# Performance work log

Measured on AMD Instinct MI355X. Metric: run time of the kernel, lower is better.

## Reference

```python
import jax, jax.numpy as jnp
import numpy as np

TAU = 0.5
EPS = 1e-12  # torch F.normalize eps
N, HIDDEN, PROJ = 16384, 512, 128


def setup_inputs() -> dict:
    key = jax.random.key(0)
    k1, k2, k3, k4 = jax.random.split(key, 4)
    scale1 = 1.0 / np.sqrt(HIDDEN)
    scale2 = 1.0 / np.sqrt(PROJ)
    return {
        "z1": jax.random.normal(k1, (N, HIDDEN), dtype=jnp.float32),
        "z2": jax.random.normal(k2, (N, HIDDEN), dtype=jnp.float32),
        "W1": jax.random.normal(k3, (HIDDEN, PROJ), dtype=jnp.float32) * scale1,
        "b1": jnp.zeros((PROJ,), dtype=jnp.float32),
        "W2": jax.random.normal(k4, (PROJ, PROJ), dtype=jnp.float32) * scale2,
        "b2": jnp.zeros((PROJ,), dtype=jnp.float32),
    }


def _project(z, W1, b1, W2, b2):
    # GRACE projection head: Linear -> ELU -> Linear
    h = jax.nn.elu(z @ W1 + b1)
    return h @ W2 + b2


def _l2_normalize(x):
    nrm = jnp.sqrt(jnp.sum(x * x, axis=1, keepdims=True))
    return x / jnp.maximum(nrm, EPS)


def _semi_loss(u, v):
    nu = _l2_normalize(u)
    nv = _l2_normalize(v)
    intra = jnp.exp((nu @ nu.T) / TAU)  # [N, N]
    inter = jnp.exp((nu @ nv.T) / TAU)  # [N, N]
    pos = jnp.diagonal(inter)
    denom = intra.sum(axis=1) + inter.sum(axis=1) - jnp.diagonal(intra)
    return -jnp.log(pos / denom)


def reference(z1, z2, W1, b1, W2, b2):
    u = _project(z1, W1, b1, W2, b2)
    v = _project(z2, W1, b1, W2, b2)
    l1 = _semi_loss(u, v)
    l2 = _semi_loss(v, u)
    return jnp.mean((l1 + l2) * 0.5)
```

## Files before the change

kernel.cpp:

```cpp
#include <hip/hip_runtime.h>

#define NROWS 16384
#define M2    32768
#define TT    128
#define HID   512
#define PROJ  128

constexpr float SCALE_L2E = 2.8853900817779268f;
constexpr float E2        = 7.38905609893065f;

typedef float f32x2   __attribute__((ext_vector_type(2)));
typedef float f32x4   __attribute__((ext_vector_type(4)));
typedef short bf16x8  __attribute__((ext_vector_type(8)));
typedef int   i32x8   __attribute__((ext_vector_type(8)));

__device__ inline short f2bf(float x) {
  union { float f; unsigned u; } v; v.f = x;
  unsigned r = v.u + 0x7fffu + ((v.u >> 16) & 1u);
  return (short)(r >> 16);
}
__device__ inline float bf2f(short s) {
  union { unsigned u; float f; } v; v.u = ((unsigned)(unsigned short)s) << 16;
  return v.f;
}
__device__ inline unsigned char f2fp8(float x) {
  return (unsigned char)(__builtin_amdgcn_cvt_pk_fp8_f32(x, x, 0, false) & 0xff);
}
__device__ inline unsigned cvtpk_bf16(float a, float b) {
  unsigned r;
  asm("v_cvt_pk_bf16_f32 %0, %1, %2" : "=v"(r) : "v"(a), "v"(b));
  return r;
}

__global__ void kprep(const float* __restrict__ W1, const float* __restrict__ W2,
                      short* __restrict__ W1t, short* __restrict__ W2t) {
  int stride = gridDim.x * blockDim.x;
  for (int idx = blockIdx.x * blockDim.x + threadIdx.x; idx < 128 * 512; idx += stride) {
    int n = idx >> 9, k = idx & 511;
    W1t[idx] = f2bf(W1[k * 128 + n]);
  }
  for (int idx = blockIdx.x * blockDim.x + threadIdx.x; idx < 128 * 128; idx += stride) {
    int n = idx >> 7, k = idx & 127;
    W2t[idx] = f2bf(W2[k * 128 + n]);
  }
}

__global__ __launch_bounds__(256) void kproj(const float* __restrict__ z1,
                                             const float* __restrict__ z2,
                                             const short* __restrict__ W1t,
                                             const float* __restrict__ b1,
                                             const short* __restrict__ W2t,
                                             const float* __restrict__ b2,
                                             short* __restrict__ nn,
                                             unsigned char* __restrict__ nnf,
                                             unsigned char* __restrict__ nsf) {
  __shared__ short hls[64 * 128];
  int wave = threadIdx.x >> 6, lane = threadIdx.x & 63;
  int lr = lane & 15, lg = lane >> 4;
  const float* z = (blockIdx.x < 256) ? z1 : z2;
  int rloc = (blockIdx.x & 255) * 64 + wave * 16;
  int rglob0 = blockIdx.x * 64 + wave * 16;
  const float* zrow = z + (size_t)(rloc + lr) * HID;

  f32x4 acc[8];
#pragma unroll
  for (int ct = 0; ct < 8; ++ct) acc[ct] = (f32x4){0.f, 0.f, 0.f, 0.f};

  for (int kc = 0; kc < HID / 32; ++kc) {
    int kof = kc * 32 + lg * 8;
    f32x4 za = *(const f32x4*)(zrow + kof);
    f32x4 zb = *(const f32x4*)(zrow + kof + 4);
    union { unsigned u[4]; bf16x8 v; } af;
    af.u[0] = cvtpk_bf16(za[0], za[1]);
    af.u[1] = cvtpk_bf16(za[2], za[3]);
    af.u[2] = cvtpk_bf16(zb[0], zb[1]);
    af.u[3] = cvtpk_bf16(zb[2], zb[3]);
#pragma unroll
    for (int ct = 0; ct < 8; ++ct) {
      bf16x8 b = *(const bf16x8*)(W1t + (ct * 16 + lr) * HID + kof);
      acc[ct] = __builtin_amdgcn_mfma_f32_16x16x32_bf16(af.v, b, acc[ct], 0, 0, 0);
    }
  }
#pragma unroll
  for (int ct = 0; ct < 8; ++ct) {
    int col = ct * 16 + lr;
    float bias = b1[col];
#pragma unroll
    for (int q = 0; q < 4; ++q) {
      int lrow = wave * 16 + lg * 4 + q;
      float x = acc[ct][q] + bias;
      x = x > 0.f ? x : (__builtin_amdgcn_exp2f(x * 1.44269504088896f) - 1.0f);
      int sw = (col >> 3) ^ (lrow & 15);
      hls[lrow * 128 + sw * 8 + (col & 7)] = f2bf(x);
    }
  }
  __syncthreads();

  int lrow2 = wave * 16 + lr;
  f32x4 acc2[8];
#pragma unroll
  for (int ct = 0; ct < 8; ++ct) acc2[ct] = (f32x4){0.f, 0.f, 0.f, 0.f};

#pragma unroll
  for (int kc = 0; kc < PROJ / 32; ++kc) {
    bf16x8 a = *(const bf16x8*)&hls[lrow2 * 128 + (((kc * 4 + lg) ^ lr) << 3)];
#pragma unroll
    for (int ct = 0; ct < 8; ++ct) {
      bf16x8 b = *(const bf16x8*)(W2t + (ct * 16 + lr) * PROJ + kc * 32 + lg * 8);
      acc2[ct] = __builtin_amdgcn_mfma_f32_16x16x32_bf16(a, b, acc2[ct], 0, 0, 0);
    }
  }
#pragma unroll
  for (int ct = 0; ct < 8; ++ct) {
    float bias = b2[ct * 16 + lr];
#pragma unroll
    for (int q = 0; q < 4; ++q) acc2[ct][q] += bias;
  }
  float inv[4];
#pragma unroll
  for (int q = 0; q < 4; ++q) {
    float s = 0.f;
#pragma unroll
    for (int ct = 0; ct < 8; ++ct) s += acc2[ct][q] * acc2[ct][q];
    s += __shfl_xor(s, 1); s += __shfl_xor(s, 2);
    s += __shfl_xor(s, 4); s += __shfl_xor(s, 8);
    inv[q] = 1.f / fmaxf(sqrtf(s), 1e-12f);
  }
#pragma unroll
  for (int ct = 0; ct < 8; ++ct) {
    int col = ct * 16 + lr;
#pragma unroll
    for (int q = 0; q < 4; ++q) {
      int row = rglob0 + lg * 4 + q;
      float v = acc2[ct][q] * inv[q];
      nn[(size_t)row * PROJ + col]  = f2bf(v);
      nnf[(size_t)row * PROJ + col] = f2fp8(v);
      nsf[(size_t)row * PROJ + col] = f2fp8(v * SCALE_L2E);
    }
  }
}

__global__ __launch_bounds__(512, 4) void ksim13(const unsigned char* __restrict__ nnf,
                                                 const unsigned char* __restrict__ nsf,
                                                 float* __restrict__ d) {
  __shared__ long BtL[256 * 16];
  __shared__ float colbuf[8][256];

  int tid = threadIdx.x;
  int w = tid >> 6, lane = tid & 63;
  int lr = lane & 15, lg = lane >> 4;

  int t = blockIdx.x;
  float ff = (float)((2 * TT + 1) * (2 * TT + 1) - 8 * t);
  int ib = (int)(((float)(2 * TT + 1) - sqrtf(ff)) * 0.5f);
  if (ib < 0) ib = 0;
  if (ib > TT - 1) ib = TT - 1;
  while (ib > 0 && ib * (2 * TT - ib + 1) / 2 > t) --ib;
  while ((ib + 1) * (2 * TT - ib) / 2 <= t) ++ib;
  int jb = ib + (t - ib * (2 * TT - ib + 1) / 2);
  bool diag = (ib == jb);

  int i0 = ib * 256 + w * 32;

  i32x8 a[2];
#pragma unroll
  for (int rb = 0; rb < 2; ++rb)
    a[rb] = *(const i32x8*)(nsf + (size_t)(i0 + rb * 16 + lr) * PROJ + lg * 32);

  {
    int slot = tid & 15, row0 = tid >> 4;
    const long* bsrc = (const long*)(nnf + (size_t)(jb * 256 + row0) * PROJ) + slot;
    long st[8];
#pragma unroll
    for (int r = 0; r < 8; ++r) st[r] = bsrc[(size_t)r * 32 * 16];
#pragma unroll
    for (int r = 0; r < 8; ++r) {
      int row = r * 32 + row0;
      BtL[row * 16 + (slot ^ (row & 15))] = st[r];
    }
  }
  __syncthreads();

  f32x4 rs0 = (f32x4){0.f, 0.f, 0.f, 0.f};
  f32x4 rs1 = (f32x4){0.f, 0.f, 0.f, 0.f};

  const char* bb = (const char*)BtL + lr * 128;
  unsigned xo0 = (unsigned)(((lg * 4 + 0) ^ lr) << 3);
  unsigned xo1 = (unsigned)(((lg * 4 + 1) ^ lr) << 3);
  unsigned xo2 = (unsigned)(((lg * 4 + 2) ^ lr) << 3);
  unsigned xo3 = (unsigned)(((lg * 4 + 3) ^ lr) << 3);

  union BFrag { long h[4]; i32x8 v; };

  BFrag cur;
  cur.h[0] = *(const long*)(bb + xo0);
  cur.h[1] = *(const long*)(bb + xo1);
  cur.h[2] = *(const long*)(bb + xo2);
  cur.h[3] = *(const long*)(bb + xo3);

#pragma unroll 2
  for (int jt = 0; jt < 16; ++jt) {
    const char* bn = bb + 2048;
    BFrag nxt;
    nxt.h[0] = *(const long*)(bn + xo0);
    nxt.h[1] = *(const long*)(bn + xo1);
    nxt.h[2] = *(const long*)(bn + xo2);
    nxt.h[3] = *(const long*)(bn + xo3);

    f32x4 c0 = (f32x4){0.f, 0.f, 0.f, 0.f};
    f32x4 c1 = (f32x4){0.f, 0.f, 0.f, 0.f};
    c0 = __builtin_amdgcn_mfma_scale_f32_16x16x128_f8f6f4(a[0], cur.v, c0, 0, 0,
                                                          0, 0x7f7f7f7f, 0, 0x7f7f7f7f);
    c1 = __builtin_amdgcn_mfma_scale_f32_16x16x128_f8f6f4(a[1], cur.v, c1, 0, 0,
                                                          0, 0x7f7f7f7f, 0, 0x7f7f7f7f);

    f32x4 e0, e1;
#pragma unroll
    for (int q = 0; q < 4; ++q) {
      e0[q] = __builtin_amdgcn_exp2f(c0[q]);
      e1[q] = __builtin_amdgcn_exp2f(c1[q]);
    }
    rs0 += e0;
    rs1 += e1;
    f32x4 s4 = e0 + e1;
    f32x2 h2 = __builtin_shufflevector(s4, s4, 0, 1)
             + __builtin_shufflevector(s4, s4, 2, 3);
    float cs = h2[0] + h2[1];
    cs += __shfl_xor(cs, 16);
    cs += __shfl_xor(cs, 32);
    if (lg == 0) colbuf[w][jt * 16 + lr] = cs;

    cur = nxt;
    bb = bn;
  }

  float myval = 0.f;
#pragma unroll
  for (int rb = 0; rb < 2; ++rb)
#pragma unroll
    for (int q = 0; q < 4; ++q) {
      float v = (rb == 0) ? rs0[q] : rs1[q];
      v += __shfl_xor(v, 1); v += __shfl_xor(v, 2);
      v += __shfl_xor(v, 4); v += __shfl_xor(v, 8);
      if (lr == rb * 4 + q) myval = v;
    }
  if (lr < 8)
    atomicAdd(&d[i0 + (lr >> 2) * 16 + lg * 4 + (lr & 3)], myval);

  __syncthreads();
  if (!diag && tid < 256) {
    float s = 0.f;
#pragma unroll
    for (int w2 = 0; w2 < 8; ++w2) s += colbuf[w2][tid];
    atomicAdd(&d[jb * 256 + tid], s);
  }
}

__global__ __launch_bounds__(256) void kfinal(const short* __restrict__ nn,
                                              const float* __restrict__ d,
                                              float* __restrict__ out) {
  int wave = threadIdx.x >> 6, lane = threadIdx.x & 63;
  int i = blockIdx.x * 256 + threadIdx.x;

  const bf16x8* a = (const bf16x8*)(nn + (size_t)i * PROJ);
  const bf16x8* b = (const bf16x8*)(nn + (size_t)(NROWS + i) * PROJ);
  float s = 0.f;
#pragma unroll
  for (int t = 0; t < PROJ / 8; ++t) {
    bf16x8 x = a[t], y = b[t];
#pragma unroll
    for (int e = 0; e < 8; ++e) s += bf2f(x[e]) * bf2f(y[e]);
  }
  float den1 = d[i] - E2;
  float den2 = d[NROWS + i] - E2;
  float li = 0.5f * (logf(den1) + logf(den2)) - s * 2.0f;

#pragma unroll
  for (int m = 1; m < 64; m <<= 1) li += __shfl_xor(li, m);
  __shared__ float ws4[4];
  if (lane == 0) ws4[wave] = li;
  __syncthreads();
  if (threadIdx.x == 0)
    atomicAdd(out, (ws4[0] + ws4[1] + ws4[2] + ws4[3]) * (1.f / (float)NROWS));
}

extern "C" void kernel_launch(void* const* d_in, const int* in_sizes, int n_in,
                              void* d_out, int out_size, void* d_ws, size_t ws_size,
                              hipStream_t stream) {
  (void)in_sizes; (void)n_in; (void)out_size; (void)ws_size;
  const float* z1 = (const float*)d_in[0];
  const float* z2 = (const float*)d_in[1];
  const float* W1 = (const float*)d_in[2];
  const float* b1 = (const float*)d_in[3];
  const float* W2 = (const float*)d_in[4];
  const float* b2 = (const float*)d_in[5];
  float* out = (float*)d_out;

  short* W1t = (short*)d_ws;
  short* W2t = W1t + 128 * 512;
  short* nn  = W2t + 128 * 128;
  unsigned char* nnf = (unsigned char*)(nn + (size_t)M2 * PROJ);
  unsigned char* nsf = nnf + (size_t)M2 * PROJ;
  float* d = (float*)(nsf + (size_t)M2 * PROJ);

  hipMemsetAsync(d_out, 0, sizeof(float), stream);
  hipMemsetAsync(d, 0, (size_t)M2 * sizeof(float), stream);

  kprep<<<16, 256, 0, stream>>>(W1, W2, W1t, W2t);
  kproj<<<M2 / 64, 256, 0, stream>>>(z1, z2, W1t, b1, W2t, b2, nn, nnf, nsf);
  ksim13<<<TT * (TT + 1) / 2, 512, 0, stream>>>(nnf, nsf, d);
  kfinal<<<NROWS / 256, 256, 0, stream>>>(nn, d, out);
}
```

Baseline: 189.0 us.

## Fuse positive-pair dot into projection kernel and software-pipeline MFMA/exp in similarity loop

The projection kernel now handles matching u and v rows in the same 512-thread block. It computes the u·v positive dot product through LDS and writes it out, so the bf16 normalized copy and the final kernel's reread of it are no longer needed. The similarity kernel is software-pipelined: the MFMA for the next tile is issued before the exp and reduction work on the previous tile, to overlap matrix and vector work. This costs extra registers and an added LDS round trip and syncs in the projection kernel.

Measured after the change: 304.7 us. 1.61x slower.

```diff
diff --git a/kernel.cpp b/kernel.cpp
--- a/kernel.cpp
+++ b/kernel.cpp
@@ -18,10 +18,6 @@
   union { float f; unsigned u; } v; v.f = x;
   unsigned r = v.u + 0x7fffu + ((v.u >> 16) & 1u);
   return (short)(r >> 16);
-}
-__device__ inline float bf2f(short s) {
-  union { unsigned u; float f; } v; v.u = ((unsigned)(unsigned short)s) << 16;
-  return v.f;
 }
 __device__ inline unsigned char f2fp8(float x) {
   return (unsigned char)(__builtin_amdgcn_cvt_pk_fp8_f32(x, x, 0, false) & 0xff);
@@ -45,22 +41,23 @@
   }
 }
 
-__global__ __launch_bounds__(256) void kproj(const float* __restrict__ z1,
+__global__ __launch_bounds__(512) void kproj(const float* __restrict__ z1,
                                              const float* __restrict__ z2,
                                              const short* __restrict__ W1t,
                                              const float* __restrict__ b1,
                                              const short* __restrict__ W2t,
                                              const float* __restrict__ b2,
-                                             short* __restrict__ nn,
                                              unsigned char* __restrict__ nnf,
-                                             unsigned char* __restrict__ nsf) {
-  __shared__ short hls[64 * 128];
+                                             unsigned char* __restrict__ nsf,
+                                             float* __restrict__ sv) {
+  __shared__ short hls[2][64 * 128];
   int wave = threadIdx.x >> 6, lane = threadIdx.x & 63;
   int lr = lane & 15, lg = lane >> 4;
-  const float* z = (blockIdx.x < 256) ? z1 : z2;
-  int rloc = (blockIdx.x & 255) * 64 + wave * 16;
-  int rglob0 = blockIdx.x * 64 + wave * 16;
-  const float* zrow = z + (size_t)(rloc + lr) * HID;
+  int uw = wave & 3, isV = wave >> 2;
+  const float* z = isV ? z2 : z1;
+  int rbase = blockIdx.x * 64 + uw * 16;
+  const float* zrow = z + (size_t)(rbase + lr) * HID;
+  short* hbase = hls[isV];
 
   f32x4 acc[8];
 #pragma unroll
@@ -87,23 +84,23 @@
     float bias = b1[col];
 #pragma unroll
     for (int q = 0; q < 4; ++q) {
-      int lrow = wave * 16 + lg * 4 + q;
+      int lrow = uw * 16 + lg * 4 + q;
       float x = acc[ct][q] + bias;
       x = x > 0.f ? x : (__builtin_amdgcn_exp2f(x * 1.44269504088896f) - 1.0f);
       int sw = (col >> 3) ^ (lrow & 15);
-      hls[lrow * 128 + sw * 8 + (col & 7)] = f2bf(x);
-    }
-  }
-  __syncthreads();
-
-  int lrow2 = wave * 16 + lr;
+      hbase[lrow * 128 + sw * 8 + (col & 7)] = f2bf(x);
+    }
+  }
+  __syncthreads();
+
+  int lrow2 = uw * 16 + lr;
   f32x4 acc2[8];
 #pragma unroll
   for (int ct = 0; ct < 8; ++ct) acc2[ct] = (f32x4){0.f, 0.f, 0.f, 0.f};
 
 #pragma unroll
   for (int kc = 0; kc < PROJ / 32; ++kc) {
-    bf16x8 a = *(const bf16x8*)&hls[lrow2 * 128 + (((kc * 4 + lg) ^ lr) << 3)];
+    bf16x8 a = *(const bf16x8*)&hbase[lrow2 * 128 + (((kc * 4 + lg) ^ lr) << 3)];
 #pragma unroll
     for (int ct = 0; ct < 8; ++ct) {
       bf16x8 b = *(const bf16x8*)(W2t + (ct * 16 + lr) * PROJ + kc * 32 + lg * 8);
@@ -126,21 +123,56 @@
     s += __shfl_xor(s, 4); s += __shfl_xor(s, 8);
     inv[q] = 1.f / fmaxf(sqrtf(s), 1e-12f);
   }
+  int rglob0 = rbase + (isV ? NROWS : 0);
 #pragma unroll
   for (int ct = 0; ct < 8; ++ct) {
     int col = ct * 16 + lr;
 #pragma unroll
     for (int q = 0; q < 4; ++q) {
+      float v = acc2[ct][q] * inv[q];
+      acc2[ct][q] = v;
       int row = rglob0 + lg * 4 + q;
-      float v = acc2[ct][q] * inv[q];
-      nn[(size_t)row * PROJ + col]  = f2bf(v);
       nnf[(size_t)row * PROJ + col] = f2fp8(v);
       nsf[(size_t)row * PROJ + col] = f2fp8(v * SCALE_L2E);
     }
   }
-}
-
-__global__ __launch_bounds__(512, 4) void ksim13(const unsigned char* __restrict__ nnf,
+
+  __syncthreads();
+  float* un = (float*)hls;
+  if (!isV) {
+#pragma unroll
+    for (int ct = 0; ct < 8; ++ct) {
+      int col = ct * 16 + lr;
+#pragma unroll
+      for (int q = 0; q < 4; ++q) {
+        int lrow = uw * 16 + lg * 4 + q;
+        un[lrow * 128 + ((col + (lrow << 2)) & 127)] = acc2[ct][q];
+      }
+    }
+  }
+  __syncthreads();
+  if (isV) {
+    float pd[4] = {0.f, 0.f, 0.f, 0.f};
+#pragma unroll
+    for (int ct = 0; ct < 8; ++ct) {
+      int col = ct * 16 + lr;
+#pragma unroll
+      for (int q = 0; q < 4; ++q) {
+        int lrow = uw * 16 + lg * 4 + q;
+        pd[q] += un[lrow * 128 + ((col + (lrow << 2)) & 127)] * acc2[ct][q];
+      }
+    }
+#pragma unroll
+    for (int q = 0; q < 4; ++q) {
+      float v = pd[q];
+      v += __shfl_xor(v, 1); v += __shfl_xor(v, 2);
+      v += __shfl_xor(v, 4); v += __shfl_xor(v, 8);
+      if (lr == 0) sv[rbase + lg * 4 + q] = v;
+    }
+  }
+}
+
+__global__ __launch_bounds__(512, 4) void ksim14(const unsigned char* __restrict__ nnf,
                                                  const unsigned char* __restrict__ nsf,
                                                  float* __restrict__ d) {
   __shared__ long BtL[256 * 16];
@@ -162,10 +194,8 @@
 
   int i0 = ib * 256 + w * 32;
 
-  i32x8 a[2];
-#pragma unroll
-  for (int rb = 0; rb < 2; ++rb)
-    a[rb] = *(const i32x8*)(nsf + (size_t)(i0 + rb * 16 + lr) * PROJ + lg * 32);
+  i32x8 a0 = *(const i32x8*)(nsf + (size_t)(i0 + lr) * PROJ + lg * 32);
+  i32x8 a1 = *(const i32x8*)(nsf + (size_t)(i0 + 16 + lr) * PROJ + lg * 32);
 
   {
     int slot = tid & 15, row0 = tid >> 4;
@@ -192,16 +222,28 @@
 
   union BFrag { long h[4]; i32x8 v; };
 
-  BFrag cur;
+  BFrag cur, nxt;
   cur.h[0] = *(const long*)(bb + xo0);
   cur.h[1] = *(const long*)(bb + xo1);
   cur.h[2] = *(const long*)(bb + xo2);
   cur.h[3] = *(const long*)(bb + xo3);
+  const char* bp = bb + 2048;
+  nxt.h[0] = *(const long*)(bp + xo0);
+  nxt.h[1] = *(const long*)(bp + xo1);
+  nxt.h[2] = *(const long*)(bp + xo2);
+  nxt.h[3] = *(const long*)(bp + xo3);
+
+  f32x4 p0 = (f32x4){0.f, 0.f, 0.f, 0.f};
+  f32x4 p1 = (f32x4){0.f, 0.f, 0.f, 0.f};
+  p0 = __builtin_amdgcn_mfma_scale_f32_16x16x128_f8f6f4(a0, cur.v, p0, 0, 0,
+                                                        0, 0x7f7f7f7f, 0, 0x7f7f7f7f);
+  p1 = __builtin_amdgcn_mfma_scale_f32_16x16x128_f8f6f4(a1, cur.v, p1, 0, 0,
+                                                        0, 0x7f7f7f7f, 0, 0x7f7f7f7f);
 
 #pragma unroll 2
-  for (int jt = 0; jt < 16; ++jt) {
-    const char* bn = bb + 2048;
-    BFrag nxt;
+  for (int jt = 1; jt < 16; ++jt) {
+    cur = nxt;
+    const char* bn = bp + 2048;
     nxt.h[0] = *(const long*)(bn + xo0);
     nxt.h[1] = *(const long*)(bn + xo1);
     nxt.h[2] = *(const long*)(bn + xo2);
@@ -209,16 +251,16 @@
 
     f32x4 c0 = (f32x4){0.f, 0.f, 0.f, 0.f};
     f32x4 c1 = (f32x4){0.f, 0.f, 0.f, 0.f};
-    c0 = __builtin_amdgcn_mfma_scale_f32_16x16x128_f8f6f4(a[0], cur.v, c0, 0, 0,
+    c0 = __builtin_amdgcn_mfma_scale_f32_16x16x128_f8f6f4(a0, cur.v, c0, 0, 0,
                                                           0, 0x7f7f7f7f, 0, 0x7f7f7f7f);
-    c1 = __builtin_amdgcn_mfma_scale_f32_16x16x128_f8f6f4(a[1], cur.v, c1, 0, 0,
+    c1 = __builtin_amdgcn_mfma_scale_f32_16x16x128_f8f6f4(a1, cur.v, c1, 0, 0,
                                                           0, 0x7f7f7f7f, 0, 0x7f7f7f7f);
 
     f32x4 e0, e1;
 #pragma unroll
     for (int q = 0; q < 4; ++q) {
-      e0[q] = __builtin_amdgcn_exp2f(c0[q]);
-      e1[q] = __builtin_amdgcn_exp2f(c1[q]);
+      e0[q] = __builtin_amdgcn_exp2f(p0[q]);
+      e1[q] = __builtin_amdgcn_exp2f(p1[q]);
     }
     rs0 += e0;
     rs1 += e1;
@@ -228,10 +270,27 @@
     float cs = h2[0] + h2[1];
     cs += __shfl_xor(cs, 16);
     cs += __shfl_xor(cs, 32);
-    if (lg == 0) colbuf[w][jt * 16 + lr] = cs;
-
-    cur = nxt;
-    bb = bn;
+    if (lg == 0) colbuf[w][(jt - 1) * 16 + lr] = cs;
+
+    p0 = c0; p1 = c1;
+    bp = bn;
+  }
+  {
+    f32x4 e0, e1;
+#pragma unroll
+    for (int q = 0; q < 4; ++q) {
+      e0[q] = __builtin_amdgcn_exp2f(p0[q]);
+      e1[q] = __builtin_amdgcn_exp2f(p1[q]);
+    }
+    rs0 += e0;
+    rs1 += e1;
+    f32x4 s4 = e0 + e1;
+    f32x2 h2 = __builtin_shufflevector(s4, s4, 0, 1)
+             + __builtin_shufflevector(s4, s4, 2, 3);
+    float cs = h2[0] + h2[1];
+    cs += __shfl_xor(cs, 16);
+    cs += __shfl_xor(cs, 32);
+    if (lg == 0) colbuf[w][15 * 16 + lr] = cs;
   }
 
   float myval = 0.f;
@@ -256,24 +315,15 @@
   }
 }
 
-__global__ __launch_bounds__(256) void kfinal(const short* __restrict__ nn,
+__global__ __launch_bounds__(256) void kfinal(const float* __restrict__ sv,
                                               const float* __restrict__ d,
                                               float* __restrict__ out) {
   int wave = threadIdx.x >> 6, lane = threadIdx.x & 63;
   int i = blockIdx.x * 256 + threadIdx.x;
 
-  const bf16x8* a = (const bf16x8*)(nn + (size_t)i * PROJ);
-  const bf16x8* b = (const bf16x8*)(nn + (size_t)(NROWS + i) * PROJ);
-  float s = 0.f;
-#pragma unroll
-  for (int t = 0; t < PROJ / 8; ++t) {
-    bf16x8 x = a[t], y = b[t];
-#pragma unroll
-    for (int e = 0; e < 8; ++e) s += bf2f(x[e]) * bf2f(y[e]);
-  }
   float den1 = d[i] - E2;
   float den2 = d[NROWS + i] - E2;
-  float li = 0.5f * (logf(den1) + logf(den2)) - s * 2.0f;
+  float li = 0.5f * (logf(den1) + logf(den2)) - sv[i] * 2.0f;
 
 #pragma unroll
   for (int m = 1; m < 64; m <<= 1) li += __shfl_xor(li, m);
@@ -298,16 +348,16 @@
 
   short* W1t = (short*)d_ws;
   short* W2t = W1t + 128 * 512;
-  short* nn  = W2t + 128 * 128;
-  unsigned char* nnf = (unsigned char*)(nn + (size_t)M2 * PROJ);
+  unsigned char* nnf = (unsigned char*)(W2t + 128 * 128);
   unsigned char* nsf = nnf + (size_t)M2 * PROJ;
-  float* d = (float*)(nsf + (size_t)M2 * PROJ);
+  float* d  = (float*)(nsf + (size_t)M2 * PROJ);
+  float* sv = d + M2;
 
   hipMemsetAsync(d_out, 0, sizeof(float), stream);
   hipMemsetAsync(d, 0, (size_t)M2 * sizeof(float), stream);
 
   kprep<<<16, 256, 0, stream>>>(W1, W2, W1t, W2t);
-  kproj<<<M2 / 64, 256, 0, stream>>>(z1, z2, W1t, b1, W2t, b2, nn, nnf, nsf);
-  ksim13<<<TT * (TT + 1) / 2, 512, 0, stream>>>(nnf, nsf, d);
-  kfinal<<<NROWS / 256, 256, 0, stream>>>(nn, d, out);
-}
+  kproj<<<NROWS / 64, 512, 0, stream>>>(z1, z2, W1t, b1, W2t, b2, nnf, nsf, sv);
+  ksim14<<<TT * (TT + 1) / 2, 512, 0, stream>>>(nnf, nsf, d);
+  kfinal<<<NROWS / 256, 256, 0, stream>>>(sv, d, out);
+}
```
